# Kernel optimization log

Measured on AMD Instinct MI355X. Metric: run time of the kernel, lower is better.

The kernel has to match this reference:

```python
import jax, jax.numpy as jnp
import numpy as np

EXTENT = 3.0            # 'radius' arg of the model is passed as extents to ContinuousConv
SEARCH_R = EXTENT / 2.0 # Open3D fixed_radius_search uses extents/2
KS = 6                  # kernel_size [6,6,6]
N, K = 10000, 32
EPS = 1e-12
FOUR_OVER_PI = float(4.0 / np.pi)


def ball_to_cube_volume_preserving(u):
    # u: [...,3] in the unit ball -> cube [-1,1]^3 (Open3D mapping:
    # MapSphereToCylinder followed by MapCylinderToCube).
    x, y, z = u[..., 0], u[..., 1], u[..., 2]
    sq = x * x + y * y + z * z
    norm = jnp.sqrt(jnp.maximum(sq, EPS))
    rho2 = x * x + y * y
    # sphere -> cylinder (volume preserving, two regions)
    in_cone = 1.25 * z * z > rho2
    s1 = jnp.sqrt(3.0 * norm / (norm + jnp.abs(z)))
    s2 = norm / jnp.sqrt(jnp.maximum(rho2, EPS))
    s = jnp.where(in_cone, s1, s2)
    xc = x * s
    yc = y * s
    zc = jnp.where(in_cone, jnp.sign(z) * norm, 1.5 * z)
    tiny = sq < EPS
    xc = jnp.where(tiny, 0.0, xc)
    yc = jnp.where(tiny, 0.0, yc)
    zc = jnp.where(tiny, 0.0, zc)
    # cylinder -> cube (inverse concentric / Shirley-Chiu map on xy disc)
    sq_xy = xc * xc + yc * yc
    norm_xy = jnp.sqrt(jnp.maximum(sq_xy, EPS))
    x_major = jnp.abs(yc) <= jnp.abs(xc)
    xd = jnp.where(jnp.abs(xc) < EPS, 1.0, xc)
    yd = jnp.where(jnp.abs(yc) < EPS, 1.0, yc)
    tx = jnp.sign(xc) * norm_xy
    ty = jnp.sign(yc) * norm_xy
    xq = jnp.where(x_major, tx, ty * FOUR_OVER_PI * jnp.arctan(xc / yd))
    yq = jnp.where(x_major, tx * FOUR_OVER_PI * jnp.arctan(yc / xd), ty)
    tiny_xy = sq_xy < EPS
    xq = jnp.where(tiny_xy, 0.0, xq)
    yq = jnp.where(tiny_xy, 0.0, yq)
    return jnp.stack([xq, yq, zc], axis=-1)


def continuous_conv(feats, pos, nidx, nmask, W, b):
    # feats [N,Cin], pos [N,3], nidx [N,K] int32 (padded), nmask [N,K] bool
    # W [KS,KS,KS,Cin,Cout], b [Cout]
    n, k = nidx.shape
    Cin, Cout = W.shape[3], W.shape[4]
    M = KS * KS * KS
    maskf = nmask.astype(feats.dtype)
    u = (pos[nidx] - pos[:, None, :]) * (2.0 / EXTENT)          # [N,K,3], unit ball
    coords = (ball_to_cube_volume_preserving(u) + 1.0) * (0.5 * (KS - 1))  # align_corners
    i0f = jnp.floor(coords)
    frac = coords - i0f
    i0 = jnp.clip(i0f.astype(jnp.int32), 0, KS - 1)
    i1 = jnp.minimum(i0 + 1, KS - 1)
    fN = feats[nidx]                                            # [N,K,Cin]
    base = jnp.arange(n, dtype=jnp.int32)[:, None] * M          # [N,1]
    # Scatter trilinear-weighted neighbor features into per-point kernel cells:
    # A[j, cell, :] = sum_{neighbors k, corners c} w_{j,k,c} * feats[nidx[j,k]]
    A = jnp.zeros((n * M, Cin), feats.dtype)
    for cx in (0, 1):
        ix = i1[..., 0] if cx else i0[..., 0]
        wx = frac[..., 0] if cx else 1.0 - frac[..., 0]
        for cy in (0, 1):
            iy = i1[..., 1] if cy else i0[..., 1]
            wy = frac[..., 1] if cy else 1.0 - frac[..., 1]
            for cz in (0, 1):
                iz = i1[..., 2] if cz else i0[..., 2]
                wz = frac[..., 2] if cz else 1.0 - frac[..., 2]
                w = wx * wy * wz * maskf                        # [N,K]
                flat = (base + (ix * KS + iy) * KS + iz).reshape(-1)
                A = A.at[flat].add((w[..., None] * fN).reshape(n * k, Cin))
    out = jnp.einsum('nmc,mco->no', A.reshape(n, M, Cin), W.reshape(M, Cin, Cout))
    # normalize=True (Open3D default): divide by neighbor count, guarded for empty
    cnt = maskf.sum(axis=1, keepdims=True)
    out = jnp.where(cnt > 0, out / jnp.maximum(cnt, 1.0), out)
    return jax.nn.relu(out + b)                                 # use_bias + activation


def setup_inputs() -> dict:
    rng = np.random.default_rng(0)
    L = 16.0  # box side -> ~32 neighbors on average within SEARCH_R
    pos = (rng.random((N, 3)) * L).astype(np.float32)
    nidx = np.zeros((N, K), np.int32)
    nmask = np.zeros((N, K), bool)
    chunk = 512
    for s in range(0, N, chunk):
        d2 = ((pos[s:s + chunk, None, :] - pos[None, :, :]) ** 2).sum(-1)
        part = np.argpartition(d2, K, axis=1)[:, :K].astype(np.int32)
        m = np.take_along_axis(d2, part, axis=1) <= SEARCH_R * SEARCH_R
        nidx[s:s + chunk] = np.where(m, part, 0)
        nmask[s:s + chunk] = m

    def p(*shape):
        return jnp.asarray((rng.standard_normal(shape) * 0.1).astype(np.float32))

    return {
        'feats': jnp.asarray(rng.standard_normal((N, 4)).astype(np.float32)),
        'pos': jnp.asarray(pos),
        'neighbor_idx': jnp.asarray(nidx),
        'neighbor_mask': jnp.asarray(nmask),
        'W1': p(KS, KS, KS, 4, 64), 'b1': jnp.zeros((64,), jnp.float32),
        'W2': p(KS, KS, KS, 64, 64), 'b2': jnp.zeros((64,), jnp.float32),
        'W3': p(KS, KS, KS, 64, 32), 'b3': jnp.zeros((32,), jnp.float32),
        'Wfc1': p(32, 64), 'bfc1': jnp.zeros((64,), jnp.float32),
        'Wfc2': p(64, 64), 'bfc2': jnp.zeros((64,), jnp.float32),
        'Wfc3': p(64, 32), 'bfc3': jnp.zeros((32,), jnp.float32),
        'Wout': p(32, 3), 'bout': jnp.zeros((3,), jnp.float32),
    }


def reference(feats, pos, neighbor_idx, neighbor_mask, W1, b1, W2, b2, W3, b3,
              Wfc1, bfc1, Wfc2, bfc2, Wfc3, bfc3, Wout, bout):
    x = continuous_conv(feats, pos, neighbor_idx, neighbor_mask, W1, b1)
    x = continuous_conv(x, pos, neighbor_idx, neighbor_mask, W2, b2)
    x = continuous_conv(x, pos, neighbor_idx, neighbor_mask, W3, b3)
    x = jax.nn.relu(x @ Wfc1 + bfc1)
    x = jax.nn.relu(x @ Wfc2 + bfc2)
    x = jax.nn.relu(x @ Wfc3 + bfc3)
    return x @ Wout + bout
```

## Files before the change

kernel.cpp:

```cpp
#include <hip/hip_runtime.h>
#include <math.h>

#define NPTS  10000
#define KNB   32
#define NCELL 216
#define NSGT  157

__device__ __forceinline__ float sgnf(float v) {
    return (v > 0.0f) ? 1.0f : ((v < 0.0f) ? -1.0f : 0.0f);
}

__device__ __forceinline__ int ld_acq(int* p) {
    return __hip_atomic_load(p, __ATOMIC_ACQUIRE, __HIP_MEMORY_SCOPE_WORKGROUP);
}
__device__ __forceinline__ void add_rel(int* p) {
    __hip_atomic_fetch_add(p, 1, __ATOMIC_RELEASE, __HIP_MEMORY_SCOPE_WORKGROUP);
}

__device__ __forceinline__ void ball_to_cube(float x, float y, float z,
                                             float& X, float& Y, float& Z) {
    const float EPSF = 1e-12f;
    const float FOPI = (float)(4.0 / 3.14159265358979323846);
    float sq   = x * x + y * y + z * z;
    float norm = sqrtf(fmaxf(sq, EPSF));
    float rho2 = x * x + y * y;
    bool in_cone = (1.25f * z * z > rho2);
    float s1 = sqrtf(3.0f * norm / (norm + fabsf(z)));
    float s2 = norm / sqrtf(fmaxf(rho2, EPSF));
    float s  = in_cone ? s1 : s2;
    float xc = x * s;
    float yc = y * s;
    float zc = in_cone ? sgnf(z) * norm : 1.5f * z;
    if (sq < EPSF) { xc = 0.0f; yc = 0.0f; zc = 0.0f; }
    float sq_xy   = xc * xc + yc * yc;
    float norm_xy = sqrtf(fmaxf(sq_xy, EPSF));
    bool x_major = (fabsf(yc) <= fabsf(xc));
    float xd = (fabsf(xc) < EPSF) ? 1.0f : xc;
    float yd = (fabsf(yc) < EPSF) ? 1.0f : yc;
    float tx = sgnf(xc) * norm_xy;
    float ty = sgnf(yc) * norm_xy;
    float xq = x_major ? tx : ty * FOPI * atanf(xc / yd);
    float yq = x_major ? tx * FOPI * atanf(yc / xd) : ty;
    if (sq_xy < EPSF) { xq = 0.0f; yq = 0.0f; }
    X = xq; Y = yq; Z = zc;
}

__global__ __launch_bounds__(256) void geom_kernel(
    const float* __restrict__ pos, const int* __restrict__ nidx,
    uint4* __restrict__ geo, float* __restrict__ cnt) {
    int t = blockIdx.x * 256 + threadIdx.x;
    if (t >= NPTS * KNB) return;
    int j = t >> 5;
    int k = t & 31;
    int nid = nidx[t];
    float px = pos[j * 3], py = pos[j * 3 + 1], pz = pos[j * 3 + 2];
    float qx = pos[nid * 3], qy = pos[nid * 3 + 1], qz = pos[nid * 3 + 2];
    float dx = __fsub_rn(px, qx), dy = __fsub_rn(py, qy), dz = __fsub_rn(pz, qz);
    float d2 = __fadd_rn(__fadd_rn(__fmul_rn(dx, dx), __fmul_rn(dy, dy)),
                         __fmul_rn(dz, dz));
    bool valid = (d2 <= 2.25f);
    if (valid && nid == 0) {
        for (int kk = 0; kk < k; ++kk) {
            if (nidx[j * KNB + kk] == 0) { valid = false; break; }
        }
    }
    uint4 g = make_uint4(0u, 0u, 0u, 0u);
    if (valid) {
        const float C = (float)(2.0 / 3.0);
        float ux = (qx - px) * C, uy = (qy - py) * C, uz = (qz - pz) * C;
        float X, Y, Z;
        ball_to_cube(ux, uy, uz, X, Y, Z);
        float cs[3] = { (X + 1.0f) * 2.5f, (Y + 1.0f) * 2.5f, (Z + 1.0f) * 2.5f };
        int i0[3], i1[3];
        float fr[3];
        #pragma unroll
        for (int d = 0; d < 3; ++d) {
            float f0 = floorf(cs[d]);
            fr[d] = cs[d] - f0;
            int a = (int)f0;
            a = min(max(a, 0), 5);
            i0[d] = a;
            i1[d] = min(a + 1, 5);
        }
        int c000 = (i0[0] * 6 + i0[1]) * 6 + i0[2];
        unsigned bits = (unsigned)c000
                      | ((unsigned)(i1[0] - i0[0]) << 8)
                      | ((unsigned)(i1[1] - i0[1]) << 9)
                      | ((unsigned)(i1[2] - i0[2]) << 10)
                      | (1u << 11)
                      | ((unsigned)nid << 12);
        g.x = __float_as_uint(fr[0]);
        g.y = __float_as_uint(fr[1]);
        g.z = __float_as_uint(fr[2]);
        g.w = bits;
        atomicAdd(&cnt[j], 1.0f);
    }
    geo[t] = g;
}

__global__ __launch_bounds__(256) void sort_kernel(
    const uint4* __restrict__ geo, uint2* __restrict__ contribs,
    int* __restrict__ starts) {
    __shared__ int hist[NCELL];
    __shared__ int pref[NCELL + 1];
    const int sg = blockIdx.x, tid = threadIdx.x;
    if (tid < NCELL) hist[tid] = 0;
    __syncthreads();
    const int npts = min(64, NPTS - sg * 64);
    const int nrec = npts * KNB;
    const uint4* gb = geo + (size_t)sg * 64 * KNB;
    for (int r = tid; r < nrec; r += 256) {
        uint4 g = gb[r];
        if (g.w & 2048u) {
            int c000 = g.w & 255u;
            int dxo = (g.w & 256u)  ? 36 : 0;
            int dyo = (g.w & 512u)  ? 6  : 0;
            int dzo = (g.w & 1024u) ? 1  : 0;
            #pragma unroll
            for (int c = 0; c < 8; ++c) {
                int cell = c000 + ((c & 4) ? dxo : 0) + ((c & 2) ? dyo : 0)
                                + ((c & 1) ? dzo : 0);
                atomicAdd(&hist[cell], 1);
            }
        }
    }
    __syncthreads();
    if (tid == 0) {
        int run = 0;
        for (int m = 0; m < NCELL; ++m) { pref[m] = run; run += hist[m]; }
        pref[NCELL] = run;
    }
    __syncthreads();
    for (int i = tid; i < NCELL + 1; i += 256)
        starts[sg * (NCELL + 1) + i] = pref[i];
    if (tid < NCELL) hist[tid] = pref[tid];
    __syncthreads();
    uint2* cb = contribs + (size_t)sg * 16384;
    for (int r = tid; r < nrec; r += 256) {
        uint4 g = gb[r];
        if (g.w & 2048u) {
            int ptl = r >> 5;
            float fx = __uint_as_float(g.x);
            float fy = __uint_as_float(g.y);
            float fz = __uint_as_float(g.z);
            int c000 = g.w & 255u;
            int dxo = (g.w & 256u)  ? 36 : 0;
            int dyo = (g.w & 512u)  ? 6  : 0;
            int dzo = (g.w & 1024u) ? 1  : 0;
            int nid = (g.w >> 12) & 16383u;
            #pragma unroll
            for (int c = 0; c < 8; ++c) {
                float wgt = ((c & 4) ? fx : 1.f - fx)
                          * ((c & 2) ? fy : 1.f - fy)
                          * ((c & 1) ? fz : 1.f - fz);
                int cell = c000 + ((c & 4) ? dxo : 0) + ((c & 2) ? dyo : 0)
                                + ((c & 1) ? dzo : 0);
                int p = atomicAdd(&hist[cell], 1);
                cb[p] = make_uint2(__float_as_uint(wgt),
                                   (unsigned)nid | ((unsigned)ptl << 14)
                                                 | ((unsigned)cell << 20));
            }
        }
    }
}

template<int CIN, int COUT, int CPC, int KSPLIT, int CO_T>
__global__ __launch_bounds__(256, 3) void conv_kernel(
    const float* __restrict__ feats, const float* __restrict__ W,
    const uint2* __restrict__ contribs, const int* __restrict__ starts,
    float* __restrict__ partial) {
    constexpr int KC   = CPC * CIN;
    constexpr int AQ   = KC / 4 + 1;
    constexpr int RD   = 2;
    constexpr int NCHUNK = NCELL / CPC;
    constexpr int NPW  = 2, NCW = 2;
    constexpr int NCOG = COUT / CO_T;
    constexpr int TPC  = CIN / 4;
    constexpr int NSLOT = 128 / TPC;
    constexpr int U    = 4;
    constexpr int Q4   = CO_T / 4;

    __shared__ float4 Ring[RD][64 * AQ];
    __shared__ int Sl[NCELL + 1];
    __shared__ int zeroc[RD], prodc[RD], consc[RD];

    const int tid  = threadIdx.x;
    const int lane = tid & 63;
    const int wave = tid >> 6;
    const int bx   = blockIdx.x;
    const int ks   = blockIdx.y;

    const int rw   = (wave + (bx & 3)) & 3;
    const bool producer = (rw >= 2);
    const int rtid = (rw & 1) * 64 + lane;

    for (int i = tid; i < NCELL + 1; i += 256)
        Sl[i] = starts[bx * (NCELL + 1) + i];
    if (tid < RD) { zeroc[tid] = 0; prodc[tid] = 0; consc[tid] = 0; }
    __syncthreads();

    const int c0 = NCHUNK * ks / KSPLIT;
    const int c1 = NCHUNK * (ks + 1) / KSPLIT;

    if (producer) {
        const int slot = rtid / TPC;
        const int ch   = rtid % TPC;
        const uint2* cbs = contribs + (size_t)bx * 16384;
        for (int c = c0; c < c1; ++c) {
            const int i = c - c0, s = i % RD, lap = i / RD;
            while (ld_acq(&consc[s]) < NCW * lap) __builtin_amdgcn_s_sleep(2);
            {
                float4 z = make_float4(0.f, 0.f, 0.f, 0.f);
                float4* dst = &Ring[s][0];
                for (int j = rtid; j < 64 * AQ; j += 128) dst[j] = z;
            }
            if (lane == 0) add_rel(&zeroc[s]);
            while (ld_acq(&zeroc[s]) < NPW * (lap + 1)) __builtin_amdgcn_s_sleep(1);
            const int cb = c * CPC;
            const int sbeg = Sl[cb], send = Sl[cb + CPC];
            float* A = (float*)&Ring[s][0];
            for (int it = sbeg + slot; it < send; it += U * NSLOT) {
                uint2 recs[U];
                #pragma unroll
                for (int u = 0; u < U; ++u)
                    recs[u] = cbs[min(it + u * NSLOT, send - 1)];
                float4 f4[U];
                #pragma unroll
                for (int u = 0; u < U; ++u)
                    f4[u] = *reinterpret_cast<const float4*>(
                        feats + (size_t)(recs[u].y & 16383) * CIN + ch * 4);
                #pragma unroll
                for (int u = 0; u < U; ++u) {
                    int idx = it + u * NSLOT;
                    if (idx < send) {
                        float wgt = __uint_as_float(recs[u].x);
                        int ptl = (recs[u].y >> 14) & 63;
                        int cel = (int)(recs[u].y >> 20);
                        float* dst = A + ptl * (AQ * 4) + (cel - cb) * CIN + ch * 4;
                        atomicAdd(dst + 0, wgt * f4[u].x);
                        atomicAdd(dst + 1, wgt * f4[u].y);
                        atomicAdd(dst + 2, wgt * f4[u].z);
                        atomicAdd(dst + 3, wgt * f4[u].w);
                    }
                }
            }
            if (lane == 0) add_rel(&prodc[s]);
        }
    } else {
        const int cog = rtid % NCOG;
        const int ptg = rtid / NCOG;
        float4 acc[4][Q4];
        #pragma unroll
        for (int p = 0; p < 4; ++p)
            #pragma unroll
            for (int q = 0; q < Q4; ++q)
                acc[p][q] = make_float4(0.f, 0.f, 0.f, 0.f);

        for (int c = c0; c < c1; ++c) {
            const int i = c - c0, s = i % RD, lap = i / RD;
            while (ld_acq(&prodc[s]) < NPW * (lap + 1)) __builtin_amdgcn_s_sleep(2);
            const float* Wc = W + (size_t)c * KC * COUT + cog * CO_T;
            const float4* Ar = &Ring[s][0];
            #pragma unroll 2
            for (int g = 0; g < KC / 4; ++g) {
                float4 wv[4][Q4];
                #pragma unroll
                for (int j = 0; j < 4; ++j) {
                    const float* wp = Wc + (size_t)(g * 4 + j) * COUT;
                    #pragma unroll
                    for (int q = 0; q < Q4; ++q)
                        wv[j][q] = *reinterpret_cast<const float4*>(wp + q * 4);
                }
                float4 av[4];
                #pragma unroll
                for (int p = 0; p < 4; ++p)
                    av[p] = Ar[(ptg + p * 16) * AQ + g];
                #pragma unroll
                for (int p = 0; p < 4; ++p) {
                    const float* ap = reinterpret_cast<const float*>(&av[p]);
                    #pragma unroll
                    for (int j = 0; j < 4; ++j) {
                        float a = ap[j];
                        #pragma unroll
                        for (int q = 0; q < Q4; ++q) {
                            acc[p][q].x = fmaf(a, wv[j][q].x, acc[p][q].x);
                            acc[p][q].y = fmaf(a, wv[j][q].y, acc[p][q].y);
                            acc[p][q].z = fmaf(a, wv[j][q].z, acc[p][q].z);
                            acc[p][q].w = fmaf(a, wv[j][q].w, acc[p][q].w);
                        }
                    }
                }
            }
            if (lane == 0) add_rel(&consc[s]);
        }

        #pragma unroll
        for (int p = 0; p < 4; ++p) {
            int n = bx * 64 + ptg + p * 16;
            if (n < NPTS) {
                float* po = partial + ((size_t)ks * NPTS + n) * COUT + cog * CO_T;
                #pragma unroll
                for (int q = 0; q < Q4; ++q)
                    *reinterpret_cast<float4*>(po + q * 4) = acc[p][q];
            }
        }
    }
}

template<int COUT, int KSPLIT>
__global__ __launch_bounds__(256) void combine_kernel(
    const float* __restrict__ partial, const float* __restrict__ cnt,
    const float* __restrict__ bias, float* __restrict__ out) {
    int idx = blockIdx.x * 256 + threadIdx.x;
    if (idx >= NPTS * COUT) return;
    int n = idx / COUT, co = idx % COUT;
    float s = 0.f;
    #pragma unroll
    for (int k2 = 0; k2 < KSPLIT; ++k2)
        s += partial[((size_t)k2 * NPTS + n) * COUT + co];
    float c = cnt[n];
    if (c > 0.f) s /= fmaxf(c, 1.f);
    out[idx] = fmaxf(s + bias[co], 0.f);
}

__global__ __launch_bounds__(64) void fc_kernel(
    const float* __restrict__ x,
    const float* __restrict__ W1, const float* __restrict__ b1,
    const float* __restrict__ W2, const float* __restrict__ b2,
    const float* __restrict__ W3, const float* __restrict__ b3,
    const float* __restrict__ W4, const float* __restrict__ b4,
    float* __restrict__ out) {
    int n = blockIdx.x;
    int lane = threadIdx.x;
    float xv = (lane < 32) ? x[(size_t)n * 32 + lane] : 0.0f;

    float t = b1[lane];
    for (int ci = 0; ci < 32; ++ci)
        t = fmaf(__shfl(xv, ci), W1[ci * 64 + lane], t);
    float h1 = fmaxf(t, 0.0f);

    t = b2[lane];
    for (int ci = 0; ci < 64; ++ci)
        t = fmaf(__shfl(h1, ci), W2[ci * 64 + lane], t);
    float h2 = fmaxf(t, 0.0f);

    int l32 = lane & 31;
    t = b3[l32];
    for (int ci = 0; ci < 64; ++ci)
        t = fmaf(__shfl(h2, ci), W3[ci * 32 + l32], t);
    float h3 = fmaxf(t, 0.0f);

    int ch = (lane < 3) ? lane : 0;
    float o = b4[ch];
    for (int ci = 0; ci < 32; ++ci)
        o = fmaf(__shfl(h3, ci), W4[ci * 3 + ch], o);
    if (lane < 3) out[(size_t)n * 3 + lane] = o;
}

extern "C" void kernel_launch(void* const* d_in, const int* in_sizes, int n_in,
                              void* d_out, int out_size, void* d_ws, size_t ws_size,
                              hipStream_t stream) {
    const float* feats = (const float*)d_in[0];
    const float* pos   = (const float*)d_in[1];
    const int*   nidx  = (const int*)d_in[2];
    const float* W1 = (const float*)d_in[4];
    const float* b1 = (const float*)d_in[5];
    const float* W2 = (const float*)d_in[6];
    const float* b2 = (const float*)d_in[7];
    const float* W3 = (const float*)d_in[8];
    const float* b3 = (const float*)d_in[9];
    const float* Wfc1 = (const float*)d_in[10];
    const float* bfc1 = (const float*)d_in[11];
    const float* Wfc2 = (const float*)d_in[12];
    const float* bfc2 = (const float*)d_in[13];
    const float* Wfc3 = (const float*)d_in[14];
    const float* bfc3 = (const float*)d_in[15];
    const float* Wout = (const float*)d_in[16];
    const float* bout = (const float*)d_in[17];

    char* ws = (char*)d_ws;
    uint2* contrib = (uint2*)(ws);
    int*   starts  = (int*)  (ws + 20578304);
    float* cnt     = (float*)(ws + 20714624);
    float* x1      = (float*)(ws + 20754624);
    float* x2      = (float*)(ws + 23314624);
    float* x3      = (float*)(ws + 25874624);
    uint4* geo     = (uint4*)(ws + 27154624);
    float* partial = (float*)(ws + 27154624);

    hipMemsetAsync(cnt, 0, NPTS * sizeof(float), stream);
    geom_kernel<<<(NPTS * KNB) / 256, 256, 0, stream>>>(pos, nidx, geo, cnt);
    sort_kernel<<<NSGT, 256, 0, stream>>>(geo, contrib, starts);

    conv_kernel<4, 64, 8, 3, 8><<<dim3(NSGT, 3), 256, 0, stream>>>(
        feats, W1, contrib, starts, partial);
    combine_kernel<64, 3><<<(NPTS * 64 + 255) / 256, 256, 0, stream>>>(
        partial, cnt, b1, x1);

    conv_kernel<64, 64, 1, 4, 8><<<dim3(NSGT, 4), 256, 0, stream>>>(
        x1, W2, contrib, starts, partial);
    combine_kernel<64, 4><<<(NPTS * 64 + 255) / 256, 256, 0, stream>>>(
        partial, cnt, b2, x2);

    conv_kernel<64, 32, 1, 4, 4><<<dim3(NSGT, 4), 256, 0, stream>>>(
        x2, W3, contrib, starts, partial);
    combine_kernel<32, 4><<<(NPTS * 32 + 255) / 256, 256, 0, stream>>>(
        partial, cnt, b3, x3);

    fc_kernel<<<NPTS, 64, 0, stream>>>(x3, Wfc1, bfc1, Wfc2, bfc2,
                                       Wfc3, bfc3, Wout, bout, (float*)d_out);
}
```

Before: 2.251 ms.

## Drop producer/consumer ring in conv, sort by cell-point, use plain stores for unique slots

New measurement: 2.200 ms. 1.02x faster.

```diff
diff --git a/kernel.cpp b/kernel.cpp
--- a/kernel.cpp
+++ b/kernel.cpp
@@ -8,13 +8,6 @@
 
 __device__ __forceinline__ float sgnf(float v) {
     return (v > 0.0f) ? 1.0f : ((v < 0.0f) ? -1.0f : 0.0f);
-}
-
-__device__ __forceinline__ int ld_acq(int* p) {
-    return __hip_atomic_load(p, __ATOMIC_ACQUIRE, __HIP_MEMORY_SCOPE_WORKGROUP);
-}
-__device__ __forceinline__ void add_rel(int* p) {
-    __hip_atomic_fetch_add(p, 1, __ATOMIC_RELEASE, __HIP_MEMORY_SCOPE_WORKGROUP);
 }
 
 __device__ __forceinline__ void ball_to_cube(float x, float y, float z,
@@ -101,10 +94,10 @@
 __global__ __launch_bounds__(256) void sort_kernel(
     const uint4* __restrict__ geo, uint2* __restrict__ contribs,
     int* __restrict__ starts) {
-    __shared__ int hist[NCELL];
-    __shared__ int pref[NCELL + 1];
+    __shared__ int hist[13824];
+    __shared__ int part[257];
     const int sg = blockIdx.x, tid = threadIdx.x;
-    if (tid < NCELL) hist[tid] = 0;
+    for (int i = tid; i < 13824; i += 256) hist[i] = 0;
     __syncthreads();
     const int npts = min(64, NPTS - sg * 64);
     const int nrec = npts * KNB;
@@ -112,6 +105,7 @@
     for (int r = tid; r < nrec; r += 256) {
         uint4 g = gb[r];
         if (g.w & 2048u) {
+            int ptl = r >> 5;
             int c000 = g.w & 255u;
             int dxo = (g.w & 256u)  ? 36 : 0;
             int dyo = (g.w & 512u)  ? 6  : 0;
@@ -120,20 +114,32 @@
             for (int c = 0; c < 8; ++c) {
                 int cell = c000 + ((c & 4) ? dxo : 0) + ((c & 2) ? dyo : 0)
                                 + ((c & 1) ? dzo : 0);
-                atomicAdd(&hist[cell], 1);
-            }
-        }
-    }
+                atomicAdd(&hist[cell * 64 + ptl], 1);
+            }
+        }
+    }
+    __syncthreads();
+    int sum = 0;
+    for (int j = 0; j < 54; ++j) sum += hist[tid * 54 + j];
+    part[tid] = sum;
     __syncthreads();
     if (tid == 0) {
         int run = 0;
-        for (int m = 0; m < NCELL; ++m) { pref[m] = run; run += hist[m]; }
-        pref[NCELL] = run;
-    }
-    __syncthreads();
-    for (int i = tid; i < NCELL + 1; i += 256)
-        starts[sg * (NCELL + 1) + i] = pref[i];
-    if (tid < NCELL) hist[tid] = pref[tid];
+        for (int i = 0; i < 256; ++i) { int v = part[i]; part[i] = run; run += v; }
+        part[256] = run;
+    }
+    __syncthreads();
+    {
+        int run = part[tid];
+        for (int j = 0; j < 54; ++j) {
+            int i = tid * 54 + j;
+            int v = hist[i]; hist[i] = run; run += v;
+        }
+    }
+    __syncthreads();
+    for (int i = tid; i < NCELL; i += 256)
+        starts[sg * (NCELL + 1) + i] = hist[i * 64];
+    if (tid == 0) starts[sg * (NCELL + 1) + NCELL] = part[256];
     __syncthreads();
     uint2* cb = contribs + (size_t)sg * 16384;
     for (int r = tid; r < nrec; r += 256) {
@@ -155,7 +161,7 @@
                           * ((c & 1) ? fz : 1.f - fz);
                 int cell = c000 + ((c & 4) ? dxo : 0) + ((c & 2) ? dyo : 0)
                                 + ((c & 1) ? dzo : 0);
-                int p = atomicAdd(&hist[cell], 1);
+                int p = atomicAdd(&hist[cell * 64 + ptl], 1);
                 cb[p] = make_uint2(__float_as_uint(wgt),
                                    (unsigned)nid | ((unsigned)ptl << 14)
                                                  | ((unsigned)cell << 20));
@@ -165,144 +171,135 @@
 }
 
 template<int CIN, int COUT, int CPC, int KSPLIT, int CO_T>
-__global__ __launch_bounds__(256, 3) void conv_kernel(
+__global__ __launch_bounds__(256, 4) void conv_kernel(
     const float* __restrict__ feats, const float* __restrict__ W,
     const uint2* __restrict__ contribs, const int* __restrict__ starts,
     float* __restrict__ partial) {
-    constexpr int KC   = CPC * CIN;
-    constexpr int AQ   = KC / 4 + 1;
-    constexpr int RD   = 2;
+    constexpr int KC    = CPC * CIN;
+    constexpr int AQ    = KC / 4 + 1;
     constexpr int NCHUNK = NCELL / CPC;
-    constexpr int NPW  = 2, NCW = 2;
-    constexpr int NCOG = COUT / CO_T;
-    constexpr int TPC  = CIN / 4;
-    constexpr int NSLOT = 128 / TPC;
-    constexpr int U    = 4;
-    constexpr int Q4   = CO_T / 4;
-
-    __shared__ float4 Ring[RD][64 * AQ];
+    constexpr int NCOG  = COUT / CO_T;
+    constexpr int NPTG  = 256 / NCOG;
+    constexpr int PT_PER = 64 / NPTG;
+    constexpr int Q4    = CO_T / 4;
+    constexpr int TPC   = CIN / 4;
+    constexpr int NSLOT = 256 / TPC;
+    constexpr int U     = 4;
+
+    __shared__ float4 A4[64 * AQ];
     __shared__ int Sl[NCELL + 1];
-    __shared__ int zeroc[RD], prodc[RD], consc[RD];
 
     const int tid  = threadIdx.x;
-    const int lane = tid & 63;
-    const int wave = tid >> 6;
     const int bx   = blockIdx.x;
     const int ks   = blockIdx.y;
-
-    const int rw   = (wave + (bx & 3)) & 3;
-    const bool producer = (rw >= 2);
-    const int rtid = (rw & 1) * 64 + lane;
+    const int cog  = tid % NCOG;
+    const int ptg  = tid / NCOG;
+    const int slot = tid / TPC;
+    const int ch   = tid % TPC;
+    const uint2* cbs = contribs + (size_t)bx * 16384;
 
     for (int i = tid; i < NCELL + 1; i += 256)
         Sl[i] = starts[bx * (NCELL + 1) + i];
-    if (tid < RD) { zeroc[tid] = 0; prodc[tid] = 0; consc[tid] = 0; }
-    __syncthreads();
 
     const int c0 = NCHUNK * ks / KSPLIT;
     const int c1 = NCHUNK * (ks + 1) / KSPLIT;
 
-    if (producer) {
-        const int slot = rtid / TPC;
-        const int ch   = rtid % TPC;
-        const uint2* cbs = contribs + (size_t)bx * 16384;
-        for (int c = c0; c < c1; ++c) {
-            const int i = c - c0, s = i % RD, lap = i / RD;
-            while (ld_acq(&consc[s]) < NCW * lap) __builtin_amdgcn_s_sleep(2);
-            {
-                float4 z = make_float4(0.f, 0.f, 0.f, 0.f);
-                float4* dst = &Ring[s][0];
-                for (int j = rtid; j < 64 * AQ; j += 128) dst[j] = z;
-            }
-            if (lane == 0) add_rel(&zeroc[s]);
-            while (ld_acq(&zeroc[s]) < NPW * (lap + 1)) __builtin_amdgcn_s_sleep(1);
-            const int cb = c * CPC;
-            const int sbeg = Sl[cb], send = Sl[cb + CPC];
-            float* A = (float*)&Ring[s][0];
-            for (int it = sbeg + slot; it < send; it += U * NSLOT) {
-                uint2 recs[U];
-                #pragma unroll
-                for (int u = 0; u < U; ++u)
-                    recs[u] = cbs[min(it + u * NSLOT, send - 1)];
-                float4 f4[U];
-                #pragma unroll
-                for (int u = 0; u < U; ++u)
-                    f4[u] = *reinterpret_cast<const float4*>(
-                        feats + (size_t)(recs[u].y & 16383) * CIN + ch * 4);
-                #pragma unroll
-                for (int u = 0; u < U; ++u) {
-                    int idx = it + u * NSLOT;
-                    if (idx < send) {
-                        float wgt = __uint_as_float(recs[u].x);
-                        int ptl = (recs[u].y >> 14) & 63;
-                        int cel = (int)(recs[u].y >> 20);
-                        float* dst = A + ptl * (AQ * 4) + (cel - cb) * CIN + ch * 4;
-                        atomicAdd(dst + 0, wgt * f4[u].x);
-                        atomicAdd(dst + 1, wgt * f4[u].y);
-                        atomicAdd(dst + 2, wgt * f4[u].z);
-                        atomicAdd(dst + 3, wgt * f4[u].w);
+    float4 acc[PT_PER][Q4];
+    #pragma unroll
+    for (int p = 0; p < PT_PER; ++p)
+        #pragma unroll
+        for (int q = 0; q < Q4; ++q)
+            acc[p][q] = make_float4(0.f, 0.f, 0.f, 0.f);
+
+    for (int c = c0; c < c1; ++c) {
+        {
+            float4 z = make_float4(0.f, 0.f, 0.f, 0.f);
+            for (int i = tid; i < 64 * AQ; i += 256) A4[i] = z;
+        }
+        __syncthreads();
+        const int cb = c * CPC;
+        const int s = Sl[cb], e = Sl[cb + CPC];
+        float* A = reinterpret_cast<float*>(A4);
+        for (int it = s + slot; it < e; it += U * NSLOT) {
+            uint2 recs[U]; unsigned pv[U], nx[U]; float4 f4[U];
+            #pragma unroll
+            for (int u = 0; u < U; ++u) {
+                int idx = min(it + u * NSLOT, e - 1);
+                recs[u] = cbs[idx];
+                pv[u] = (idx > 0) ? cbs[idx - 1].y : 0xFFFFFFFFu;
+                nx[u] = cbs[idx + 1].y;
+            }
+            #pragma unroll
+            for (int u = 0; u < U; ++u)
+                f4[u] = *reinterpret_cast<const float4*>(
+                    feats + (size_t)(recs[u].y & 16383) * CIN + ch * 4);
+            #pragma unroll
+            for (int u = 0; u < U; ++u) {
+                int idx = it + u * NSLOT;
+                if (idx < e) {
+                    unsigned y = recs[u].y;
+                    unsigned key = y >> 14;
+                    bool dup = ((pv[u] >> 14) == key) || ((nx[u] >> 14) == key);
+                    float wgt = __uint_as_float(recs[u].x);
+                    int ptl = (int)(key & 63u);
+                    int cel = (int)(y >> 20);
+                    float* dst = A + ptl * (AQ * 4) + (cel - cb) * CIN + ch * 4;
+                    float vx = wgt * f4[u].x, vy = wgt * f4[u].y;
+                    float vz = wgt * f4[u].z, vw = wgt * f4[u].w;
+                    if (!dup) {
+                        *reinterpret_cast<float4*>(dst) = make_float4(vx, vy, vz, vw);
+                    } else {
+                        atomicAdd(dst + 0, vx);
+                        atomicAdd(dst + 1, vy);
+                        atomicAdd(dst + 2, vz);
+                        atomicAdd(dst + 3, vw);
                     }
                 }
             }
-            if (lane == 0) add_rel(&prodc[s]);
-        }
-    } else {
-        const int cog = rtid % NCOG;
-        const int ptg = rtid / NCOG;
-        float4 acc[4][Q4];
-        #pragma unroll
-        for (int p = 0; p < 4; ++p)
-            #pragma unroll
-            for (int q = 0; q < Q4; ++q)
-                acc[p][q] = make_float4(0.f, 0.f, 0.f, 0.f);
-
-        for (int c = c0; c < c1; ++c) {
-            const int i = c - c0, s = i % RD, lap = i / RD;
-            while (ld_acq(&prodc[s]) < NPW * (lap + 1)) __builtin_amdgcn_s_sleep(2);
-            const float* Wc = W + (size_t)c * KC * COUT + cog * CO_T;
-            const float4* Ar = &Ring[s][0];
-            #pragma unroll 2
-            for (int g = 0; g < KC / 4; ++g) {
-                float4 wv[4][Q4];
+        }
+        __syncthreads();
+        const float* Wc = W + (size_t)c * KC * COUT + cog * CO_T;
+        #pragma unroll 2
+        for (int g = 0; g < KC / 4; ++g) {
+            float4 wv[4][Q4];
+            #pragma unroll
+            for (int j = 0; j < 4; ++j) {
+                const float* wp = Wc + (size_t)(g * 4 + j) * COUT;
+                #pragma unroll
+                for (int q = 0; q < Q4; ++q)
+                    wv[j][q] = *reinterpret_cast<const float4*>(wp + q * 4);
+            }
+            float4 av[PT_PER];
+            #pragma unroll
+            for (int p = 0; p < PT_PER; ++p)
+                av[p] = A4[(ptg + p * NPTG) * AQ + g];
+            #pragma unroll
+            for (int p = 0; p < PT_PER; ++p) {
+                const float* ap = reinterpret_cast<const float*>(&av[p]);
                 #pragma unroll
                 for (int j = 0; j < 4; ++j) {
-                    const float* wp = Wc + (size_t)(g * 4 + j) * COUT;
+                    float a = ap[j];
                     #pragma unroll
-                    for (int q = 0; q < Q4; ++q)
-                        wv[j][q] = *reinterpret_cast<const float4*>(wp + q * 4);
-                }
-                float4 av[4];
-                #pragma unroll
-                for (int p = 0; p < 4; ++p)
-                    av[p] = Ar[(ptg + p * 16) * AQ + g];
-                #pragma unroll
-                for (int p = 0; p < 4; ++p) {
-                    const float* ap = reinterpret_cast<const float*>(&av[p]);
-                    #pragma unroll
-                    for (int j = 0; j < 4; ++j) {
-                        float a = ap[j];
-                        #pragma unroll
-                        for (int q = 0; q < Q4; ++q) {
-                            acc[p][q].x = fmaf(a, wv[j][q].x, acc[p][q].x);
-                            acc[p][q].y = fmaf(a, wv[j][q].y, acc[p][q].y);
-                            acc[p][q].z = fmaf(a, wv[j][q].z, acc[p][q].z);
-                            acc[p][q].w = fmaf(a, wv[j][q].w, acc[p][q].w);
-                        }
+                    for (int q = 0; q < Q4; ++q) {
+                        acc[p][q].x = fmaf(a, wv[j][q].x, acc[p][q].x);
+                        acc[p][q].y = fmaf(a, wv[j][q].y, acc[p][q].y);
+                        acc[p][q].z = fmaf(a, wv[j][q].z, acc[p][q].z);
+                        acc[p][q].w = fmaf(a, wv[j][q].w, acc[p][q].w);
                     }
                 }
             }
-            if (lane == 0) add_rel(&consc[s]);
-        }
-
-        #pragma unroll
-        for (int p = 0; p < 4; ++p) {
-            int n = bx * 64 + ptg + p * 16;
-            if (n < NPTS) {
-                float* po = partial + ((size_t)ks * NPTS + n) * COUT + cog * CO_T;
-                #pragma unroll
-                for (int q = 0; q < Q4; ++q)
-                    *reinterpret_cast<float4*>(po + q * 4) = acc[p][q];
-            }
+        }
+        __syncthreads();
+    }
+
+    #pragma unroll
+    for (int p = 0; p < PT_PER; ++p) {
+        int n = bx * 64 + ptg + p * NPTG;
+        if (n < NPTS) {
+            float* po = partial + ((size_t)ks * NPTS + n) * COUT + cog * CO_T;
+            #pragma unroll
+            for (int q = 0; q < Q4; ++q)
+                *reinterpret_cast<float4*>(po + q * 4) = acc[p][q];
         }
     }
 }
@@ -388,23 +385,32 @@
     uint4* geo     = (uint4*)(ws + 27154624);
     float* partial = (float*)(ws + 27154624);
 
+    const bool big = ws_size >= (size_t)(27154624 + 6 * 2560000);
+
     hipMemsetAsync(cnt, 0, NPTS * sizeof(float), stream);
     geom_kernel<<<(NPTS * KNB) / 256, 256, 0, stream>>>(pos, nidx, geo, cnt);
     sort_kernel<<<NSGT, 256, 0, stream>>>(geo, contrib, starts);
 
-    conv_kernel<4, 64, 8, 3, 8><<<dim3(NSGT, 3), 256, 0, stream>>>(
+    conv_kernel<4, 64, 8, 4, 8><<<dim3(NSGT, 4), 256, 0, stream>>>(
         feats, W1, contrib, starts, partial);
-    combine_kernel<64, 3><<<(NPTS * 64 + 255) / 256, 256, 0, stream>>>(
+    combine_kernel<64, 4><<<(NPTS * 64 + 255) / 256, 256, 0, stream>>>(
         partial, cnt, b1, x1);
 
-    conv_kernel<64, 64, 1, 4, 8><<<dim3(NSGT, 4), 256, 0, stream>>>(
-        x1, W2, contrib, starts, partial);
-    combine_kernel<64, 4><<<(NPTS * 64 + 255) / 256, 256, 0, stream>>>(
-        partial, cnt, b2, x2);
-
-    conv_kernel<64, 32, 1, 4, 4><<<dim3(NSGT, 4), 256, 0, stream>>>(
+    if (big) {
+        conv_kernel<64, 64, 1, 6, 8><<<dim3(NSGT, 6), 256, 0, stream>>>(
+            x1, W2, contrib, starts, partial);
+        combine_kernel<64, 6><<<(NPTS * 64 + 255) / 256, 256, 0, stream>>>(
+            partial, cnt, b2, x2);
+    } else {
+        conv_kernel<64, 64, 1, 4, 8><<<dim3(NSGT, 4), 256, 0, stream>>>(
+            x1, W2, contrib, starts, partial);
+        combine_kernel<64, 4><<<(NPTS * 64 + 255) / 256, 256, 0, stream>>>(
+            partial, cnt, b2, x2);
+    }
+
+    conv_kernel<64, 32, 1, 6, 4><<<dim3(NSGT, 6), 256, 0, stream>>>(
         x2, W3, contrib, starts, partial);
-    combine_kernel<32, 4><<<(NPTS * 32 + 255) / 256, 256, 0, stream>>>(
+    combine_kernel<32, 6><<<(NPTS * 32 + 255) / 256, 256, 0, stream>>>(
         partial, cnt, b3, x3);
 
     fc_kernel<<<NPTS, 64, 0, stream>>>(x3, Wfc1, bfc1, Wfc2, bfc2,
```
